# Kernel tuning notes

Hardware: AMD Instinct MI355X
Metric: run time of the kernel (lower is better)

## Reference

```python
import jax, jax.numpy as jnp
import numpy as np

BN_EPS = 1e-5

def _square_distance(a, b):
    # a: (B,N,3), b: (B,M,3) -> (B,N,M) squared euclidean distance
    a2 = jnp.sum(a * a, axis=-1)[:, :, None]
    b2 = jnp.sum(b * b, axis=-1)[:, None, :]
    return a2 + b2 - 2.0 * jnp.einsum('bnd,bmd->bnm', a, b)

def _bn(x, gamma, beta, mean, var):
    # eval-mode batchnorm over channel (last) dim
    return (x - mean) * jax.lax.rsqrt(var + BN_EPS) * gamma + beta

def setup_inputs() -> dict:
    key = jax.random.key(0)
    ks = jax.random.split(key, 16)
    B, M, N, D, C = 4, 2048, 16384, 64, 64
    din, dout = C + D, 64
    return {
        'xyz_down': jax.random.normal(ks[0], (B, M, 3), jnp.float32),
        'xyz_up': jax.random.normal(ks[1], (B, N, 3), jnp.float32),
        'feat_down': jax.random.normal(ks[2], (B, M, D), jnp.float32),
        'feat_up': jax.random.normal(ks[3], (B, N, C), jnp.float32),
        'W1': jax.random.normal(ks[4], (din, din), jnp.float32) * 0.05,
        'b1': jax.random.normal(ks[5], (din,), jnp.float32) * 0.05,
        'bn1_gamma': jax.random.uniform(ks[6], (din,), jnp.float32, 0.5, 1.5),
        'bn1_beta': jax.random.normal(ks[7], (din,), jnp.float32) * 0.05,
        'bn1_mean': jax.random.normal(ks[8], (din,), jnp.float32) * 0.05,
        'bn1_var': jax.random.uniform(ks[9], (din,), jnp.float32, 0.5, 1.5),
        'W2': jax.random.normal(ks[10], (dout, din), jnp.float32) * 0.05,
        'b2': jax.random.normal(ks[11], (dout,), jnp.float32) * 0.05,
        'bn2_gamma': jax.random.uniform(ks[12], (dout,), jnp.float32, 0.5, 1.5),
        'bn2_beta': jax.random.normal(ks[13], (dout,), jnp.float32) * 0.05,
        'bn2_mean': jax.random.normal(ks[14], (dout,), jnp.float32) * 0.05,
        'bn2_var': jax.random.uniform(ks[15], (dout,), jnp.float32, 0.5, 1.5),
    }

def reference(xyz_down, xyz_up, feat_down, feat_up,
              W1, b1, bn1_gamma, bn1_beta, bn1_mean, bn1_var,
              W2, b2, bn2_gamma, bn2_beta, bn2_mean, bn2_var):
    dist = _square_distance(xyz_up, xyz_down)              # (B,N,M)
    dist_recip = 1.0 / (dist + 1e-8)
    weight = dist_recip / jnp.sum(dist_recip, axis=2, keepdims=True)
    # bmm-equivalent of the original broadcast-multiply-sum
    feat_interp = jnp.einsum('bnm,bmd->bnd', weight, feat_down)  # (B,N,D)
    x = jnp.concatenate([feat_up, feat_interp], axis=-1)   # (B,N,C+D)
    # Conv1d(k=1) == pointwise linear over channel dim
    x = jnp.einsum('bnc,oc->bno', x, W1) + b1
    x = jax.nn.relu(_bn(x, bn1_gamma, bn1_beta, bn1_mean, bn1_var))
    x = jnp.einsum('bnc,oc->bno', x, W2) + b2
    x = _bn(x, bn2_gamma, bn2_beta, bn2_mean, bn2_var)
    return x
```

## Files before the change

### kernel.cpp

```cpp
#include <hip/hip_runtime.h>

typedef unsigned short u16;
typedef unsigned int   u32;
typedef unsigned long long u64;

typedef __attribute__((ext_vector_type(8))) short bf16x8;
typedef __attribute__((ext_vector_type(4))) float f32x4;
typedef __attribute__((ext_vector_type(2))) float f32x2;

#define BB 4
#define MM 2048
#define NN 16384
#define DD 64

__device__ __forceinline__ u16 f2bf(float f) {
    union { float f; u32 u; } v; v.f = f;
    u32 r = v.u + 0x7fffu + ((v.u >> 16) & 1u);
    return (u16)(r >> 16);
}

__device__ __forceinline__ u32 pack_trunc(float hi, float lo) {
    union { float f; u32 u; } a, b; a.f = hi; b.f = lo;
    return __builtin_amdgcn_perm(a.u, b.u, 0x07060302);
}

__device__ __forceinline__ u32 pack_rne(float hi, float lo) {
    return (u32)f2bf(lo) | ((u32)f2bf(hi) << 16);
}

__device__ __forceinline__ bf16x8 pack8(float4 p, float4 q) {
    bf16x8 v;
    v[0] = (short)f2bf(p.x); v[1] = (short)f2bf(p.y);
    v[2] = (short)f2bf(p.z); v[3] = (short)f2bf(p.w);
    v[4] = (short)f2bf(q.x); v[5] = (short)f2bf(q.y);
    v[6] = (short)f2bf(q.z); v[7] = (short)f2bf(q.w);
    return v;
}

#define OFF_FDT   0ull
#define OFF_XYZP  1048576ull
#define OFF_W1S   1179648ull
#define OFF_W2S   1212416ull
#define OFF_BN    1228800ull
#define WS_NEED   1230336ull

__global__ __launch_bounds__(256)
void prep7_kernel(const float* __restrict__ xyz_down,
                  const float* __restrict__ feat_down,
                  const float* __restrict__ W1, const float* __restrict__ b1,
                  const float* __restrict__ g1, const float* __restrict__ be1,
                  const float* __restrict__ m1, const float* __restrict__ v1,
                  const float* __restrict__ W2, const float* __restrict__ b2,
                  const float* __restrict__ g2, const float* __restrict__ be2,
                  const float* __restrict__ m2, const float* __restrict__ v2,
                  u16* __restrict__ fdT, float4* __restrict__ xyzP,
                  u16* __restrict__ w1s, u16* __restrict__ w2s,
                  float* __restrict__ bnbuf)
{
    const int blk = blockIdx.x, t = threadIdx.x;
    if (blk < 256) {
        __shared__ u16 T[32 * 72];
        const int b = blk >> 6, mt = blk & 63;
        const int c = mt >> 1, h = mt & 1;
        {
            const int row = t >> 3, seg = (t & 7) * 8;
            const float4* src = (const float4*)(feat_down + ((size_t)(b * MM + mt * 32 + row)) * 64 + seg);
            float4 v0 = src[0], v1 = src[1];
            bf16x8 pk = pack8(v0, v1);
            *(bf16x8*)&T[row * 72 + seg] = pk;
        }
        __syncthreads();
        {
            const int dt = t >> 6, lane = t & 63;
            const int q = lane >> 4, nl = lane & 15;
            union { u16 hh[8]; uint4 qq; } o;
#pragma unroll
            for (int j = 0; j < 8; j++) o.hh[j] = T[(q * 8 + j) * 72 + dt * 16 + nl];
            *(uint4*)&fdT[(size_t)(b * 64 + c * 2 + h) * 2048 + dt * 512 + lane * 8] = o.qq;
        }
    } else if (blk < 272) {
        int g = (blk - 256) * 256 + t;
        int b = g >> 10, p = g & 1023;
        const float* s = xyz_down + ((size_t)b * MM + 2 * p) * 3;
        float x0 = s[0], y0 = s[1], z0 = s[2];
        float x1 = s[3], y1 = s[4], z1 = s[5];
        float w0 = x0 * x0 + y0 * y0 + z0 * z0 + 1e-8f;
        float w1v = x1 * x1 + y1 * y1 + z1 * z1 + 1e-8f;
        xyzP[(size_t)g * 2 + 0] = make_float4(-2.f * x0, -2.f * x1, -2.f * y0, -2.f * y1);
        xyzP[(size_t)g * 2 + 1] = make_float4(-2.f * z0, -2.f * z1, w0, w1v);
    } else if (blk < 280) {
        int slot = (blk - 272) * 256 + t;
        int f = slot >> 6, l = slot & 63;
        int kg = f >> 3, ot = f & 7;
        int o = ot * 16 + (l & 15), c = kg * 32 + (l >> 4) * 8;
        const float4* src = (const float4*)(W1 + (size_t)o * 128 + c);
        bf16x8 v = pack8(src[0], src[1]);
        *(bf16x8*)&w1s[(size_t)slot * 8] = v;
    } else if (blk < 284) {
        int slot = (blk - 280) * 256 + t;
        int f = slot >> 6, l = slot & 63;
        int kg = f >> 2, ot = f & 3;
        int o = ot * 16 + (l & 15), c = kg * 32 + (l >> 4) * 8;
        const float4* src = (const float4*)(W2 + (size_t)o * 128 + c);
        bf16x8 v = pack8(src[0], src[1]);
        *(bf16x8*)&w2s[(size_t)slot * 8] = v;
    } else {
        if (t < 128) {
            float a = g1[t] * rsqrtf(v1[t] + 1e-5f);
            bnbuf[t] = a;
            bnbuf[128 + t] = (b1[t] - m1[t]) * a + be1[t];
        } else if (t < 192) {
            int o = t - 128;
            float a = g2[o] * rsqrtf(v2[o] + 1e-5f);
            bnbuf[256 + o] = a;
            bnbuf[320 + o] = (b2[o] - m2[o]) * a + be2[o];
        }
    }
}

__global__ __launch_bounds__(512, 4)
void fused12_kernel(const float* __restrict__ xyz_up,
                    const u16* __restrict__ fdT,
                    const float4* __restrict__ xyzP,
                    const float* __restrict__ feat_up,
                    const u16* __restrict__ w1s,
                    const u16* __restrict__ w2s,
                    const float* __restrict__ bnbuf,
                    float* __restrict__ out)
{
    __shared__ __align__(16) char smem[34816];
    __shared__ float bnl[384];
    float4* const xzA = (float4*)smem;
    float4* const xzB = (float4*)smem + 1024;
    u16*   const xh   = (u16*)smem;
    float* const of   = (float*)smem;

    const int tid  = threadIdx.x;
    const int b    = blockIdx.x >> 7;
    const int n0   = (blockIdx.x & 127) * 128;
    const int wave = tid >> 6;
    const int lane = tid & 63;
    const int q    = lane >> 4;
    const int nl   = lane & 15;
    const int rg   = wave & 3;
    const int h    = wave >> 2;

    if (tid < 384) bnl[tid] = bnbuf[tid];

    {
        const float4* src = xyzP + (size_t)b * 2048;
#pragma unroll
        for (int k = 0; k < 4; k++) {
            int idx = tid + k * 512;
            float4 v = src[idx];
            int pair = idx >> 1;
            if (idx & 1) xzB[pair] = v; else xzA[pair] = v;
        }
    }

    float ax[2], ay[2], az[2];
    f32x2 a22[2];
#pragma unroll
    for (int rt = 0; rt < 2; rt++) {
        const int row = n0 + rg * 32 + rt * 16 + nl;
        const float* xu = xyz_up + ((size_t)(b * NN + row)) * 3;
        ax[rt] = xu[0]; ay[rt] = xu[1]; az[rt] = xu[2];
        float a2 = ax[rt] * ax[rt] + ay[rt] * ay[rt] + az[rt] * az[rt];
        a22[rt] = (f32x2){a2, a2};
    }
    const f32x2 eps2 = (f32x2){1e-8f, 1e-8f};

    f32x4 acc[2][4];
#pragma unroll
    for (int rt = 0; rt < 2; rt++)
#pragma unroll
        for (int i = 0; i < 4; i++) acc[rt][i] = (f32x4){0.f, 0.f, 0.f, 0.f};
    f32x4 accd[2];
    accd[0] = (f32x4){0.f, 0.f, 0.f, 0.f};
    accd[1] = (f32x4){0.f, 0.f, 0.f, 0.f};

    bf16x8 ones;
#pragma unroll
    for (int i = 0; i < 8; i++) ones[i] = (short)0x3F80;

    const u16* fdbW = fdT + (size_t)(b * 64 + h) * 2048 + (size_t)lane * 8;

    bf16x8 bbc[4], bbn[4];
#pragma unroll
    for (int dt = 0; dt < 4; dt++)
        bbc[dt] = *(const bf16x8*)(fdbW + dt * 512);

    __syncthreads();

    for (int c = 0; c < 32; ++c) {
        if (c + 1 < 32) {
#pragma unroll
            for (int dt = 0; dt < 4; dt++)
                bbn[dt] = *(const bf16x8*)(fdbW + (size_t)(c + 1) * 4096 + dt * 512);
        }

        u32 fr[2][4];
#pragma unroll
        for (int jp = 0; jp < 4; jp++) {
            const int pi = c * 32 + h * 16 + q * 4 + jp;
            float4 ld0 = xzA[pi];
            float4 ld1 = xzB[pi];
            f32x2 px = (f32x2){ld0.x, ld0.y};
            f32x2 py = (f32x2){ld0.z, ld0.w};
            f32x2 pz = (f32x2){ld1.x, ld1.y};
            f32x2 pw = (f32x2){ld1.z, ld1.w};
#pragma unroll
            for (int rt = 0; rt < 2; rt++) {
                f32x2 d = __builtin_elementwise_fma(px, (f32x2){ax[rt], ax[rt]},
                          __builtin_elementwise_fma(py, (f32x2){ay[rt], ay[rt]},
                          __builtin_elementwise_fma(pz, (f32x2){az[rt], az[rt]},
                                                    pw + a22[rt])));
                d = __builtin_elementwise_max(d, eps2);
                float r0 = __builtin_amdgcn_rcpf(d.x);
                float r1 = __builtin_amdgcn_rcpf(d.y);
                fr[rt][jp] = pack_trunc(r1, r0);
            }
        }
#pragma unroll
        for (int rt = 0; rt < 2; rt++) {
            union { u32 u[4]; bf16x8 v; } af;
            af.u[0] = fr[rt][0]; af.u[1] = fr[rt][1];
            af.u[2] = fr[rt][2]; af.u[3] = fr[rt][3];
#pragma unroll
            for (int dt = 0; dt < 4; dt++)
                acc[rt][dt] = __builtin_amdgcn_mfma_f32_16x16x32_bf16(af.v, bbc[dt], acc[rt][dt], 0, 0, 0);
            accd[rt] = __builtin_amdgcn_mfma_f32_16x16x32_bf16(af.v, ones, accd[rt], 0, 0, 0);
        }
#pragma unroll
        for (int dt = 0; dt < 4; dt++) bbc[dt] = bbn[dt];
    }

    const int fur = tid >> 2, fsg = (tid & 3) * 16;
    const float4* fup = (const float4*)(feat_up + ((size_t)(b * NN + n0 + fur)) * 64 + fsg);
    float4 f0 = fup[0], f1 = fup[1], f2 = fup[2], f3 = fup[3];

    __syncthreads();

    if (h) {
#pragma unroll
        for (int rt = 0; rt < 2; rt++)
#pragma unroll
        for (int reg = 0; reg < 4; reg++) {
            int row = rg * 32 + rt * 16 + q * 4 + reg;
#pragma unroll
            for (int dt = 0; dt < 4; dt++)
                of[row * 68 + dt * 16 + nl] = acc[rt][dt][reg];
            if (nl == 0) of[row * 68 + 64] = accd[rt][reg];
        }
    }
    __syncthreads();
    if (!h) {
#pragma unroll
        for (int rt = 0; rt < 2; rt++)
#pragma unroll
        for (int reg = 0; reg < 4; reg++) {
            int row = rg * 32 + rt * 16 + q * 4 + reg;
#pragma unroll
            for (int dt = 0; dt < 4; dt++)
                acc[rt][dt][reg] += of[row * 68 + dt * 16 + nl];
            accd[rt][reg] += of[row * 68 + 64];
        }
    }
    __syncthreads();
    if (!h) {
#pragma unroll
        for (int rt = 0; rt < 2; rt++)
#pragma unroll
        for (int reg = 0; reg < 4; reg++) {
            float inv = 1.0f / accd[rt][reg];
            int row = rg * 32 + rt * 16 + q * 4 + reg;
#pragma unroll
            for (int dt = 0; dt < 4; dt++)
                xh[row * 136 + 64 + dt * 16 + nl] = f2bf(acc[rt][dt][reg] * inv);
        }
    }
    {
        uint4 o0, o1;
        o0.x = pack_rne(f0.y, f0.x); o0.y = pack_rne(f0.w, f0.z);
        o0.z = pack_rne(f1.y, f1.x); o0.w = pack_rne(f1.w, f1.z);
        o1.x = pack_rne(f2.y, f2.x); o1.y = pack_rne(f2.w, f2.z);
        o1.z = pack_rne(f3.y, f3.x); o1.w = pack_rne(f3.w, f3.z);
        uint4* xd = (uint4*)&xh[fur * 136 + fsg];
        xd[0] = o0; xd[1] = o1;
    }
    __syncthreads();

    f32x4 acc1[8];
#pragma unroll
    for (int i = 0; i < 8; i++) acc1[i] = (f32x4){0.f, 0.f, 0.f, 0.f};
#pragma unroll
    for (int kg = 0; kg < 4; kg++) {
        bf16x8 afr = *(bf16x8*)&xh[(wave * 16 + nl) * 136 + kg * 32 + q * 8];
#pragma unroll
        for (int ot = 0; ot < 8; ot++) {
            bf16x8 bf = *(const bf16x8*)(w1s + ((size_t)(kg * 8 + ot) * 64 + lane) * 8);
            acc1[ot] = __builtin_amdgcn_mfma_f32_16x16x32_bf16(afr, bf, acc1[ot], 0, 0, 0);
        }
    }
#pragma unroll
    for (int ot = 0; ot < 8; ot++) {
        int o = ot * 16 + nl;
        float aa = bnl[o], bc = bnl[128 + o];
#pragma unroll
        for (int reg = 0; reg < 4; reg++) {
            float v = fmaxf(fmaf(acc1[ot][reg], aa, bc), 0.f);
            xh[(wave * 16 + q * 4 + reg) * 136 + o] = f2bf(v);
        }
    }

    f32x4 acc2[4];
#pragma unroll
    for (int i = 0; i < 4; i++) acc2[i] = (f32x4){0.f, 0.f, 0.f, 0.f};
#pragma unroll
    for (int kg = 0; kg < 4; kg++) {
        bf16x8 afr = *(bf16x8*)&xh[(wave * 16 + nl) * 136 + kg * 32 + q * 8];
#pragma unroll
        for (int ot = 0; ot < 4; ot++) {
            bf16x8 bf = *(const bf16x8*)(w2s + ((size_t)(kg * 4 + ot) * 64 + lane) * 8);
            acc2[ot] = __builtin_amdgcn_mfma_f32_16x16x32_bf16(afr, bf, acc2[ot], 0, 0, 0);
        }
    }
#pragma unroll
    for (int ot = 0; ot < 4; ot++) {
        int o = ot * 16 + nl;
        float aa = bnl[256 + o], bc = bnl[320 + o];
#pragma unroll
        for (int reg = 0; reg < 4; reg++)
            of[(wave * 16 + q * 4 + reg) * 68 + o] = fmaf(acc2[ot][reg], aa, bc);
    }

    {
        const float4* sf = (const float4*)&of[fur * 68 + fsg];
        float4* dst = (float4*)(out + ((size_t)(b * NN + n0 + fur)) * 64 + fsg);
#pragma unroll
        for (int i = 0; i < 4; i++) dst[i] = sf[i];
    }
}

#define TN 128
#define BM 64
#define RS 72
#define FS 72

__global__ __launch_bounds__(256, 3)
void interp_kernel(const float* __restrict__ xyz_down,
                   const float* __restrict__ xyz_up,
                   const float* __restrict__ feat_down,
                   u16* __restrict__ interp_out)
{
    __shared__ u16   rbuf[TN * RS];
    __shared__ u16   ftbuf[DD * FS];
    __shared__ float xyzb[BM * 3];
    __shared__ float denp[TN * 2];
    __shared__ float invden[TN];

    const int tid = threadIdx.x;
    const int b  = blockIdx.x >> 7;
    const int n0 = (blockIdx.x & 127) * TN;

    const int nl_r = tid >> 1;
    const int half = tid & 1;
    const float* xu = xyz_up + (size_t)(b * NN + n0 + nl_r) * 3;
    const float ax = xu[0], ay = xu[1], az = xu[2];

    denp[tid] = 0.f;

    const int wave = tid >> 6;
    const int lane = tid & 63;
    const int q    = lane >> 4;
    const int nl   = lane & 15;

    f32x4 acc[2][4];
#pragma unroll
    for (int i = 0; i < 2; i++)
#pragma unroll
        for (int j = 0; j < 4; j++) acc[i][j] = (f32x4){0.f, 0.f, 0.f, 0.f};

    const int sm = (tid & 31) * 2;
    const int sd = (tid >> 5) * 8;

    for (int mc = 0; mc < MM; mc += BM) {
        __syncthreads();
        if (tid < 192) xyzb[tid] = xyz_down[(size_t)(b * MM + mc) * 3 + tid];
        {
            const float4* f0 = (const float4*)(feat_down + (size_t)(b * MM + mc + sm) * DD + sd);
            const float4* f1 = (const float4*)(feat_down + (size_t)(b * MM + mc + sm + 1) * DD + sd);
            float4 a0 = f0[0], a1 = f0[1];
            float4 b0 = f1[0], b1 = f1[1];
            float r0[8] = {a0.x, a0.y, a0.z, a0.w, a1.x, a1.y, a1.z, a1.w};
            float r1[8] = {b0.x, b0.y, b0.z, b0.w, b1.x, b1.y, b1.z, b1.w};
#pragma unroll
            for (int j = 0; j < 8; j++) {
                u32 pk = (u32)f2bf(r0[j]) | ((u32)f2bf(r1[j]) << 16);
                *(u32*)&ftbuf[(sd + j) * FS + sm] = pk;
            }
        }
        __syncthreads();
        {
            float dlc = 0.f;
#pragma unroll
            for (int s = 0; s < 4; s++) {
                bf16x8 v;
#pragma unroll
                for (int j = 0; j < 8; j++) {
                    int m = half * 32 + s * 8 + j;
                    float dx = ax - xyzb[3 * m + 0];
                    float dy = ay - xyzb[3 * m + 1];
                    float dz = az - xyzb[3 * m + 2];
                    float d = fmaf(dx, dx, fmaf(dy, dy, dz * dz)) + 1e-8f;
                    float r = __builtin_amdgcn_rcpf(d);
                    dlc += r;
                    v[j] = (short)f2bf(r);
                }
                *(bf16x8*)&rbuf[nl_r * RS + half * 32 + s * 8] = v;
            }
            denp[nl_r * 2 + half] += dlc;
        }
        __syncthreads();
        {
            const int rowbase = wave * 32;
#pragma unroll
            for (int k0 = 0; k0 < BM; k0 += 32) {
                bf16x8 a0 = *(bf16x8*)&rbuf[(rowbase + nl) * RS + k0 + q * 8];
                bf16x8 a1 = *(bf16x8*)&rbuf[(rowbase + 16 + nl) * RS + k0 + q * 8];
#pragma unroll
                for (int dt = 0; dt < 4; dt++) {
                    bf16x8 bb = *(bf16x8*)&ftbuf[(dt * 16 + nl) * FS + k0 + q * 8];
                    acc[0][dt] = __builtin_amdgcn_mfma_f32_16x16x32_bf16(a0, bb, acc[0][dt], 0, 0, 0);
                    acc[1][dt] = __builtin_amdgcn_mfma_f32_16x16x32_bf16(a1, bb, acc[1][dt], 0, 0, 0);
                }
            }
        }
    }

    __syncthreads();
    if (tid < TN) invden[tid] = 1.0f / (denp[tid * 2] + denp[tid * 2 + 1]);
    __syncthreads();
    {
        const int rowbase = wave * 32;
#pragma unroll
        for (int nt = 0; nt < 2; nt++) {
#pragma unroll
            for (int reg = 0; reg < 4; reg++) {
                int nloc = rowbase + nt * 16 + q * 4 + reg;
                float inv = invden[nloc];
                size_t gbase = (size_t)(b * NN + n0 + nloc) * DD;
#pragma unroll
                for (int dt = 0; dt < 4; dt++)
                    interp_out[gbase + dt * 16 + nl] = f2bf(acc[nt][dt][reg] * inv);
            }
        }
    }
}

#define T2 64

__global__ __launch_bounds__(256, 1)
void mlp_kernel(const float* __restrict__ feat_up,
                const u16*   __restrict__ interp,
                const float* __restrict__ W1, const float* __restrict__ b1,
                const float* __restrict__ g1, const float* __restrict__ be1,
                const float* __restrict__ m1, const float* __restrict__ v1,
                const float* __restrict__ W2, const float* __restrict__ b2,
                const float* __restrict__ g2, const float* __restrict__ be2,
                const float* __restrict__ m2, const float* __restrict__ v2,
                float* __restrict__ out)
{
    __shared__ u16 xb[T2 * 136];
    __shared__ u16 hb[T2 * 136];
    __shared__ u16 w1b[128 * 136];
    __shared__ u16 w2b[64 * 136];
    __shared__ float A1[128], Bc1[128], A2[64], Bc2[64];

    const int tid = threadIdx.x;
    const int b  = blockIdx.x >> 8;
    const int n0 = (blockIdx.x & 255) * T2;
    const int wave = tid >> 6;
    const int lane = tid & 63;
    const int q    = lane >> 4;
    const int nl   = lane & 15;

    if (tid < 128) {
        float a = g1[tid] * rsqrtf(v1[tid] + 1e-5f);
        A1[tid]  = a;
        Bc1[tid] = (b1[tid] - m1[tid]) * a + be1[tid];
    } else if (tid < 192) {
        int o = tid - 128;
        float a = g2[o] * rsqrtf(v2[o] + 1e-5f);
        A2[o]  = a;
        Bc2[o] = (b2[o] - m2[o]) * a + be2[o];
    }
    {
        const float4* src = (const float4*)(W1 + (size_t)(tid >> 1) * 128 + (tid & 1) * 64);
        u16* dst = &w1b[(tid >> 1) * 136 + (tid & 1) * 64];
#pragma unroll
        for (int i = 0; i < 8; i++)
            *(bf16x8*)(dst + 8 * i) = pack8(src[2 * i], src[2 * i + 1]);
    }
    {
        const float4* src = (const float4*)(W2 + (size_t)(tid >> 2) * 128 + (tid & 3) * 32);
        u16* dst = &w2b[(tid >> 2) * 136 + (tid & 3) * 32];
#pragma unroll
        for (int i = 0; i < 4; i++)
            *(bf16x8*)(dst + 8 * i) = pack8(src[2 * i], src[2 * i + 1]);
    }
    if (tid < 128) {
        int n = tid >> 1, hf = tid & 1;
        const float4* src = (const float4*)(feat_up + (size_t)(b * NN + n0 + n) * 64 + hf * 32);
        u16* dst = &xb[n * 136 + hf * 32];
#pragma unroll
        for (int i = 0; i < 4; i++)
            *(bf16x8*)(dst + 8 * i) = pack8(src[2 * i], src[2 * i + 1]);
    } else {
        int t2 = tid - 128;
        int n = t2 >> 1, hf = t2 & 1;
        const uint4* src = (const uint4*)(interp + (size_t)(b * NN + n0 + n) * 64 + hf * 32);
        u16* dst = &xb[n * 136 + 64 + hf * 32];
#pragma unroll
        for (int i = 0; i < 4; i++)
            *(uint4*)(dst + 8 * i) = src[i];
    }
    __syncthreads();

    f32x4 acc1[8];
#pragma unroll
    for (int i = 0; i < 8; i++) acc1[i] = (f32x4){0.f, 0.f, 0.f, 0.f};
#pragma unroll
    for (int k0 = 0; k0 < 128; k0 += 32) {
        bf16x8 a = *(bf16x8*)&xb[(wave * 16 + nl) * 136 + k0 + q * 8];
#pragma unroll
        for (int ot = 0; ot < 8; ot++) {
            bf16x8 bb = *(bf16x8*)&w1b[(ot * 16 + nl) * 136 + k0 + q * 8];
            acc1[ot] = __builtin_amdgcn_mfma_f32_16x16x32_bf16(a, bb, acc1[ot], 0, 0, 0);
        }
    }
#pragma unroll
    for (int ot = 0; ot < 8; ot++) {
        int o = ot * 16 + nl;
        float aa = A1[o], bc = Bc1[o];
#pragma unroll
        for (int reg = 0; reg < 4; reg++) {
            float v = fmaxf(fmaf(acc1[ot][reg], aa, bc), 0.f);
            hb[(wave * 16 + q * 4 + reg) * 136 + o] = f2bf(v);
        }
    }
    __syncthreads();

    f32x4 acc2[4];
#pragma unroll
    for (int i = 0; i < 4; i++) acc2[i] = (f32x4){0.f, 0.f, 0.f, 0.f};
#pragma unroll
    for (int k0 = 0; k0 < 128; k0 += 32) {
        bf16x8 a = *(bf16x8*)&hb[(wave * 16 + nl) * 136 + k0 + q * 8];
#pragma unroll
        for (int ot = 0; ot < 4; ot++) {
            bf16x8 bb = *(bf16x8*)&w2b[(ot * 16 + nl) * 136 + k0 + q * 8];
            acc2[ot] = __builtin_amdgcn_mfma_f32_16x16x32_bf16(a, bb, acc2[ot], 0, 0, 0);
        }
    }
#pragma unroll
    for (int ot = 0; ot < 4; ot++) {
        int o = ot * 16 + nl;
        float aa = A2[o], bc = Bc2[o];
#pragma unroll
        for (int reg = 0; reg < 4; reg++)
            out[(size_t)(b * NN + n0 + wave * 16 + q * 4 + reg) * 64 + o] =
                fmaf(acc2[ot][reg], aa, bc);
    }
}

extern "C" void kernel_launch(void* const* d_in, const int* in_sizes, int n_in,
                              void* d_out, int out_size, void* d_ws, size_t ws_size,
                              hipStream_t stream) {
    const float* xyz_down  = (const float*)d_in[0];
    const float* xyz_up    = (const float*)d_in[1];
    const float* feat_down = (const float*)d_in[2];
    const float* feat_up   = (const float*)d_in[3];
    const float* W1  = (const float*)d_in[4];
    const float* b1  = (const float*)d_in[5];
    const float* g1  = (const float*)d_in[6];
    const float* be1 = (const float*)d_in[7];
    const float* m1  = (const float*)d_in[8];
    const float* v1  = (const float*)d_in[9];
    const float* W2  = (const float*)d_in[10];
    const float* b2  = (const float*)d_in[11];
    const float* g2  = (const float*)d_in[12];
    const float* be2 = (const float*)d_in[13];
    const float* m2  = (const float*)d_in[14];
    const float* v2  = (const float*)d_in[15];
    float* out = (float*)d_out;
    char* ws = (char*)d_ws;

    if (ws_size >= WS_NEED) {
        u16*    fdT   = (u16*)(ws + OFF_FDT);
        float4* xyzP  = (float4*)(ws + OFF_XYZP);
        u16*    w1s   = (u16*)(ws + OFF_W1S);
        u16*    w2s   = (u16*)(ws + OFF_W2S);
        float*  bnbuf = (float*)(ws + OFF_BN);

        prep7_kernel<<<dim3(285), dim3(256), 0, stream>>>(
            xyz_down, feat_down, W1, b1, g1, be1, m1, v1,
            W2, b2, g2, be2, m2, v2, fdT, xyzP, w1s, w2s, bnbuf);
        fused12_kernel<<<dim3(BB * (NN / 128)), dim3(512), 0, stream>>>(
            xyz_up, fdT, xyzP, feat_up, w1s, w2s, bnbuf, out);
    } else {
        u16* interp = (u16*)d_ws;
        interp_kernel<<<dim3(BB * (NN / TN)), dim3(256), 0, stream>>>(
            xyz_down, xyz_up, feat_down, interp);
        mlp_kernel<<<dim3(BB * (NN / T2)), dim3(256), 0, stream>>>(
            feat_up, interp, W1, b1, g1, be1, m1, v1,
            W2, b2, g2, be2, m2, v2, out);
    }
}
```

Measured before the change: 140.1 us.

## Double per-block row tile to 256 and unroll fdT chunk loop by two

Each block now handles 256 query points instead of 128, so each wave computes four 16-row tiles against the shared xyz_down and feat_down fragments. Every fdT B-fragment and every xyz LDS load is reused across twice as many rows. The distance loop is unrolled by two chunks with a prefetch of the next pair. The cost is much higher register and LDS use (launch bounds drop to 2 blocks, shared memory doubles) and half as many blocks, 256 in total, which may underfill the GPU's CUs.

Result: no change. 142.9 us (+2.0%).

```diff
diff --git a/kernel.cpp b/kernel.cpp
--- a/kernel.cpp
+++ b/kernel.cpp
@@ -118,8 +118,8 @@
     }
 }
 
-__global__ __launch_bounds__(512, 4)
-void fused12_kernel(const float* __restrict__ xyz_up,
+__global__ __launch_bounds__(512, 2)
+void fused13_kernel(const float* __restrict__ xyz_up,
                     const u16* __restrict__ fdT,
                     const float4* __restrict__ xyzP,
                     const float* __restrict__ feat_up,
@@ -128,7 +128,7 @@
                     const float* __restrict__ bnbuf,
                     float* __restrict__ out)
 {
-    __shared__ __align__(16) char smem[34816];
+    __shared__ __align__(16) char smem[69632];
     __shared__ float bnl[384];
     float4* const xzA = (float4*)smem;
     float4* const xzB = (float4*)smem + 1024;
@@ -136,14 +136,15 @@
     float* const of   = (float*)smem;
 
     const int tid  = threadIdx.x;
-    const int b    = blockIdx.x >> 7;
-    const int n0   = (blockIdx.x & 127) * 128;
+    const int b    = blockIdx.x >> 6;
+    const int n0   = (blockIdx.x & 63) * 256;
     const int wave = tid >> 6;
     const int lane = tid & 63;
     const int q    = lane >> 4;
     const int nl   = lane & 15;
     const int rg   = wave & 3;
     const int h    = wave >> 2;
+    const int wb   = rg * 64;
 
     if (tid < 384) bnl[tid] = bnbuf[tid];
 
@@ -158,11 +159,11 @@
         }
     }
 
-    float ax[2], ay[2], az[2];
-    f32x2 a22[2];
-#pragma unroll
-    for (int rt = 0; rt < 2; rt++) {
-        const int row = n0 + rg * 32 + rt * 16 + nl;
+    float ax[4], ay[4], az[4];
+    f32x2 a22[4];
+#pragma unroll
+    for (int rt = 0; rt < 4; rt++) {
+        const int row = n0 + wb + rt * 16 + nl;
         const float* xu = xyz_up + ((size_t)(b * NN + row)) * 3;
         ax[rt] = xu[0]; ay[rt] = xu[1]; az[rt] = xu[2];
         float a2 = ax[rt] * ax[rt] + ay[rt] * ay[rt] + az[rt] * az[rt];
@@ -170,14 +171,14 @@
     }
     const f32x2 eps2 = (f32x2){1e-8f, 1e-8f};
 
-    f32x4 acc[2][4];
-#pragma unroll
-    for (int rt = 0; rt < 2; rt++)
+    f32x4 acc[4][4];
+#pragma unroll
+    for (int rt = 0; rt < 4; rt++)
 #pragma unroll
         for (int i = 0; i < 4; i++) acc[rt][i] = (f32x4){0.f, 0.f, 0.f, 0.f};
-    f32x4 accd[2];
-    accd[0] = (f32x4){0.f, 0.f, 0.f, 0.f};
-    accd[1] = (f32x4){0.f, 0.f, 0.f, 0.f};
+    f32x4 accd[4];
+#pragma unroll
+    for (int rt = 0; rt < 4; rt++) accd[rt] = (f32x4){0.f, 0.f, 0.f, 0.f};
 
     bf16x8 ones;
 #pragma unroll
@@ -185,68 +186,83 @@
 
     const u16* fdbW = fdT + (size_t)(b * 64 + h) * 2048 + (size_t)lane * 8;
 
-    bf16x8 bbc[4], bbn[4];
-#pragma unroll
-    for (int dt = 0; dt < 4; dt++)
-        bbc[dt] = *(const bf16x8*)(fdbW + dt * 512);
-
-    __syncthreads();
-
-    for (int c = 0; c < 32; ++c) {
-        if (c + 1 < 32) {
-#pragma unroll
-            for (int dt = 0; dt < 4; dt++)
-                bbn[dt] = *(const bf16x8*)(fdbW + (size_t)(c + 1) * 4096 + dt * 512);
-        }
-
-        u32 fr[2][4];
-#pragma unroll
-        for (int jp = 0; jp < 4; jp++) {
-            const int pi = c * 32 + h * 16 + q * 4 + jp;
-            float4 ld0 = xzA[pi];
-            float4 ld1 = xzB[pi];
-            f32x2 px = (f32x2){ld0.x, ld0.y};
-            f32x2 py = (f32x2){ld0.z, ld0.w};
-            f32x2 pz = (f32x2){ld1.x, ld1.y};
-            f32x2 pw = (f32x2){ld1.z, ld1.w};
-#pragma unroll
-            for (int rt = 0; rt < 2; rt++) {
-                f32x2 d = __builtin_elementwise_fma(px, (f32x2){ax[rt], ax[rt]},
-                          __builtin_elementwise_fma(py, (f32x2){ay[rt], ay[rt]},
-                          __builtin_elementwise_fma(pz, (f32x2){az[rt], az[rt]},
-                                                    pw + a22[rt])));
-                d = __builtin_elementwise_max(d, eps2);
-                float r0 = __builtin_amdgcn_rcpf(d.x);
-                float r1 = __builtin_amdgcn_rcpf(d.y);
-                fr[rt][jp] = pack_trunc(r1, r0);
+    bf16x8 A[4], B[4];
+#pragma unroll
+    for (int dt = 0; dt < 4; dt++) {
+        A[dt] = *(const bf16x8*)(fdbW + dt * 512);
+        B[dt] = *(const bf16x8*)(fdbW + 4096 + dt * 512);
+    }
+
+    __syncthreads();
+
+#define DIST_MFMA(CIDX, BBUF)                                                  \
+    {                                                                          \
+        u32 fr[4][4];                                                          \
+        _Pragma("unroll")                                                      \
+        for (int jp = 0; jp < 4; jp++) {                                       \
+            const int pi = (CIDX) * 32 + h * 16 + q * 4 + jp;                  \
+            float4 ld0 = xzA[pi];                                              \
+            float4 ld1 = xzB[pi];                                              \
+            f32x2 px = (f32x2){ld0.x, ld0.y};                                  \
+            f32x2 py = (f32x2){ld0.z, ld0.w};                                  \
+            f32x2 pz = (f32x2){ld1.x, ld1.y};                                  \
+            f32x2 pw = (f32x2){ld1.z, ld1.w};                                  \
+            _Pragma("unroll")                                                  \
+            for (int rt = 0; rt < 4; rt++) {                                   \
+                f32x2 d = __builtin_elementwise_fma(px, (f32x2){ax[rt], ax[rt]},\
+                          __builtin_elementwise_fma(py, (f32x2){ay[rt], ay[rt]},\
+                          __builtin_elementwise_fma(pz, (f32x2){az[rt], az[rt]},\
+                                                    pw + a22[rt])));           \
+                d = __builtin_elementwise_max(d, eps2);                        \
+                float r0 = __builtin_amdgcn_rcpf(d.x);                         \
+                float r1 = __builtin_amdgcn_rcpf(d.y);                         \
+                fr[rt][jp] = pack_trunc(r1, r0);                               \
+            }                                                                  \
+        }                                                                      \
+        _Pragma("unroll")                                                      \
+        for (int rt = 0; rt < 4; rt++) {                                       \
+            union { u32 u[4]; bf16x8 v; } af;                                  \
+            af.u[0] = fr[rt][0]; af.u[1] = fr[rt][1];                          \
+            af.u[2] = fr[rt][2]; af.u[3] = fr[rt][3];                          \
+            _Pragma("unroll")                                                  \
+            for (int dt = 0; dt < 4; dt++)                                     \
+                acc[rt][dt] = __builtin_amdgcn_mfma_f32_16x16x32_bf16(af.v, (BBUF)[dt], acc[rt][dt], 0, 0, 0); \
+            accd[rt] = __builtin_amdgcn_mfma_f32_16x16x32_bf16(af.v, ones, accd[rt], 0, 0, 0); \
+        }                                                                      \
+    }
+
+    for (int cc = 0; cc < 16; ++cc) {
+        bf16x8 nA[4], nB[4];
+        if (cc < 15) {
+            const u16* base = fdbW + (size_t)(2 * cc + 2) * 4096;
+#pragma unroll
+            for (int dt = 0; dt < 4; dt++) {
+                nA[dt] = *(const bf16x8*)(base + dt * 512);
+                nB[dt] = *(const bf16x8*)(base + 4096 + dt * 512);
             }
         }
-#pragma unroll
-        for (int rt = 0; rt < 2; rt++) {
-            union { u32 u[4]; bf16x8 v; } af;
-            af.u[0] = fr[rt][0]; af.u[1] = fr[rt][1];
-            af.u[2] = fr[rt][2]; af.u[3] = fr[rt][3];
-#pragma unroll
-            for (int dt = 0; dt < 4; dt++)
-                acc[rt][dt] = __builtin_amdgcn_mfma_f32_16x16x32_bf16(af.v, bbc[dt], acc[rt][dt], 0, 0, 0);
-            accd[rt] = __builtin_amdgcn_mfma_f32_16x16x32_bf16(af.v, ones, accd[rt], 0, 0, 0);
-        }
-#pragma unroll
-        for (int dt = 0; dt < 4; dt++) bbc[dt] = bbn[dt];
-    }
-
-    const int fur = tid >> 2, fsg = (tid & 3) * 16;
+        DIST_MFMA(2 * cc,     A);
+        DIST_MFMA(2 * cc + 1, B);
+        if (cc < 15) {
+#pragma unroll
+            for (int dt = 0; dt < 4; dt++) { A[dt] = nA[dt]; B[dt] = nB[dt]; }
+        }
+    }
+#undef DIST_MFMA
+
+    const int fur = tid >> 1, fsg = (tid & 1) * 32;
     const float4* fup = (const float4*)(feat_up + ((size_t)(b * NN + n0 + fur)) * 64 + fsg);
     float4 f0 = fup[0], f1 = fup[1], f2 = fup[2], f3 = fup[3];
+    float4 f4 = fup[4], f5 = fup[5], f6 = fup[6], f7 = fup[7];
 
     __syncthreads();
 
     if (h) {
 #pragma unroll
-        for (int rt = 0; rt < 2; rt++)
+        for (int rt = 0; rt < 4; rt++)
 #pragma unroll
         for (int reg = 0; reg < 4; reg++) {
-            int row = rg * 32 + rt * 16 + q * 4 + reg;
+            int row = wb + rt * 16 + q * 4 + reg;
 #pragma unroll
             for (int dt = 0; dt < 4; dt++)
                 of[row * 68 + dt * 16 + nl] = acc[rt][dt][reg];
@@ -256,10 +272,10 @@
     __syncthreads();
     if (!h) {
 #pragma unroll
-        for (int rt = 0; rt < 2; rt++)
+        for (int rt = 0; rt < 4; rt++)
 #pragma unroll
         for (int reg = 0; reg < 4; reg++) {
-            int row = rg * 32 + rt * 16 + q * 4 + reg;
+            int row = wb + rt * 16 + q * 4 + reg;
 #pragma unroll
             for (int dt = 0; dt < 4; dt++)
                 acc[rt][dt][reg] += of[row * 68 + dt * 16 + nl];
@@ -269,37 +285,47 @@
     __syncthreads();
     if (!h) {
 #pragma unroll
-        for (int rt = 0; rt < 2; rt++)
+        for (int rt = 0; rt < 4; rt++)
 #pragma unroll
         for (int reg = 0; reg < 4; reg++) {
             float inv = 1.0f / accd[rt][reg];
-            int row = rg * 32 + rt * 16 + q * 4 + reg;
+            int row = wb + rt * 16 + q * 4 + reg;
 #pragma unroll
             for (int dt = 0; dt < 4; dt++)
                 xh[row * 136 + 64 + dt * 16 + nl] = f2bf(acc[rt][dt][reg] * inv);
         }
     }
     {
-        uint4 o0, o1;
+        uint4 o0, o1, o2, o3;
         o0.x = pack_rne(f0.y, f0.x); o0.y = pack_rne(f0.w, f0.z);
         o0.z = pack_rne(f1.y, f1.x); o0.w = pack_rne(f1.w, f1.z);
         o1.x = pack_rne(f2.y, f2.x); o1.y = pack_rne(f2.w, f2.z);
         o1.z = pack_rne(f3.y, f3.x); o1.w = pack_rne(f3.w, f3.z);
+        o2.x = pack_rne(f4.y, f4.x); o2.y = pack_rne(f4.w, f4.z);
+        o2.z = pack_rne(f5.y, f5.x); o2.w = pack_rne(f5.w, f5.z);
+        o3.x = pack_rne(f6.y, f6.x); o3.y = pack_rne(f6.w, f6.z);
+        o3.z = pack_rne(f7.y, f7.x); o3.w = pack_rne(f7.w, f7.z);
         uint4* xd = (uint4*)&xh[fur * 136 + fsg];
-        xd[0] = o0; xd[1] = o1;
-    }
-    __syncthreads();
-
-    f32x4 acc1[8];
-#pragma unroll
-    for (int i = 0; i < 8; i++) acc1[i] = (f32x4){0.f, 0.f, 0.f, 0.f};
+        xd[0] = o0; xd[1] = o1; xd[2] = o2; xd[3] = o3;
+    }
+    __syncthreads();
+
+    f32x4 acc1[2][8];
+#pragma unroll
+    for (int st = 0; st < 2; st++)
+#pragma unroll
+        for (int i = 0; i < 8; i++) acc1[st][i] = (f32x4){0.f, 0.f, 0.f, 0.f};
 #pragma unroll
     for (int kg = 0; kg < 4; kg++) {
-        bf16x8 afr = *(bf16x8*)&xh[(wave * 16 + nl) * 136 + kg * 32 + q * 8];
+        bf16x8 afr[2];
+#pragma unroll
+        for (int st = 0; st < 2; st++)
+            afr[st] = *(bf16x8*)&xh[(wave * 32 + st * 16 + nl) * 136 + kg * 32 + q * 8];
 #pragma unroll
         for (int ot = 0; ot < 8; ot++) {
             bf16x8 bf = *(const bf16x8*)(w1s + ((size_t)(kg * 8 + ot) * 64 + lane) * 8);
-            acc1[ot] = __builtin_amdgcn_mfma_f32_16x16x32_bf16(afr, bf, acc1[ot], 0, 0, 0);
+            acc1[0][ot] = __builtin_amdgcn_mfma_f32_16x16x32_bf16(afr[0], bf, acc1[0][ot], 0, 0, 0);
+            acc1[1][ot] = __builtin_amdgcn_mfma_f32_16x16x32_bf16(afr[1], bf, acc1[1][ot], 0, 0, 0);
         }
     }
 #pragma unroll
@@ -307,22 +333,30 @@
         int o = ot * 16 + nl;
         float aa = bnl[o], bc = bnl[128 + o];
 #pragma unroll
+        for (int st = 0; st < 2; st++)
+#pragma unroll
         for (int reg = 0; reg < 4; reg++) {
-            float v = fmaxf(fmaf(acc1[ot][reg], aa, bc), 0.f);
-            xh[(wave * 16 + q * 4 + reg) * 136 + o] = f2bf(v);
-        }
-    }
-
-    f32x4 acc2[4];
-#pragma unroll
-    for (int i = 0; i < 4; i++) acc2[i] = (f32x4){0.f, 0.f, 0.f, 0.f};
+            float v = fmaxf(fmaf(acc1[st][ot][reg], aa, bc), 0.f);
+            xh[(wave * 32 + st * 16 + q * 4 + reg) * 136 + o] = f2bf(v);
+        }
+    }
+
+    f32x4 acc2[2][4];
+#pragma unroll
+    for (int st = 0; st < 2; st++)
+#pragma unroll
+        for (int i = 0; i < 4; i++) acc2[st][i] = (f32x4){0.f, 0.f, 0.f, 0.f};
 #pragma unroll
     for (int kg = 0; kg < 4; kg++) {
-        bf16x8 afr = *(bf16x8*)&xh[(wave * 16 + nl) * 136 + kg * 32 + q * 8];
+        bf16x8 afr[2];
+#pragma unroll
+        for (int st = 0; st < 2; st++)
+            afr[st] = *(bf16x8*)&xh[(wave * 32 + st * 16 + nl) * 136 + kg * 32 + q * 8];
 #pragma unroll
         for (int ot = 0; ot < 4; ot++) {
             bf16x8 bf = *(const bf16x8*)(w2s + ((size_t)(kg * 4 + ot) * 64 + lane) * 8);
-            acc2[ot] = __builtin_amdgcn_mfma_f32_16x16x32_bf16(afr, bf, acc2[ot], 0, 0, 0);
+            acc2[0][ot] = __builtin_amdgcn_mfma_f32_16x16x32_bf16(afr[0], bf, acc2[0][ot], 0, 0, 0);
+            acc2[1][ot] = __builtin_amdgcn_mfma_f32_16x16x32_bf16(afr[1], bf, acc2[1][ot], 0, 0, 0);
         }
     }
 #pragma unroll
@@ -330,15 +364,19 @@
         int o = ot * 16 + nl;
         float aa = bnl[256 + o], bc = bnl[320 + o];
 #pragma unroll
+        for (int st = 0; st < 2; st++)
+#pragma unroll
         for (int reg = 0; reg < 4; reg++)
-            of[(wave * 16 + q * 4 + reg) * 68 + o] = fmaf(acc2[ot][reg], aa, bc);
+            of[(wave * 32 + st * 16 + q * 4 + reg) * 68 + o] = fmaf(acc2[st][ot][reg], aa, bc);
     }
 
     {
-        const float4* sf = (const float4*)&of[fur * 68 + fsg];
-        float4* dst = (float4*)(out + ((size_t)(b * NN + n0 + fur)) * 64 + fsg);
-#pragma unroll
-        for (int i = 0; i < 4; i++) dst[i] = sf[i];
+        const int rr = lane >> 1, sg = (lane & 1) * 32;
+        const int r = wave * 32 + rr;
+        const float4* sf = (const float4*)&of[r * 68 + sg];
+        float4* dst = (float4*)(out + ((size_t)(b * NN + n0 + r)) * 64 + sg);
+#pragma unroll
+        for (int i = 0; i < 8; i++) dst[i] = sf[i];
     }
 }
 
@@ -606,7 +644,7 @@
         prep7_kernel<<<dim3(285), dim3(256), 0, stream>>>(
             xyz_down, feat_down, W1, b1, g1, be1, m1, v1,
             W2, b2, g2, be2, m2, v2, fdT, xyzP, w1s, w2s, bnbuf);
-        fused12_kernel<<<dim3(BB * (NN / 128)), dim3(512), 0, stream>>>(
+        fused13_kernel<<<dim3(BB * (NN / 256)), dim3(512), 0, stream>>>(
             xyz_up, fdT, xyzP, feat_up, w1s, w2s, bnbuf, out);
     } else {
         u16* interp = (u16*)d_ws;
```
